# Kernel tuning notes

Hardware: AMD Instinct MI355X
Metric: run time of the kernel (lower is better)

The kernel has to match this reference:

```python
import jax, jax.numpy as jnp
import numpy as np
from jax import lax

N, C, H, W = 32, 256, 56, 56
SHIFT = 2  # p_5_1_0, frozen random.randint(-3,3)

def setup_inputs() -> dict:
    key = jax.random.key(0)
    k1, k2, k3 = jax.random.split(key, 3)
    x = jax.random.normal(k1, (N, C, H, W), dtype=jnp.float32)
    w6 = jax.random.normal(k2, (C, 1), dtype=jnp.float32) * 0.1  # trunc_normal(std=0.1) approx
    w7 = jax.random.normal(k3, (C, C * 25), dtype=jnp.float32) * (1.0 / np.sqrt(C * 25))
    return {"x": x, "w6": w6, "w7": w7}

def reference(x, w6, w7):
    # t_1: max over width -> (n,c,h)
    t1 = jnp.max(x, axis=3)
    # t_3/t_4: relu then tanh
    t4 = jnp.tanh(jax.nn.relu(x))
    # t_5: roll along height axis
    t5 = jnp.roll(x, SHIFT, axis=2)
    # t_6: einsum 'abcd,be->aecd' with e=1 -> (n,h,w)
    t6 = jnp.einsum('nchw,c->nhw', t4, w6[:, 0])
    # t_2 + p_7: unfold(5x5, dilation=3, padding=6) + 1x1 conv == dilated 5x5 conv.
    # unfold channel ordering is c*25 + (kh*5+kw), so reshape to OIHW directly.
    conv_w = w7.reshape(C, C, 5, 5)
    t7 = lax.conv_general_dilated(
        x, conv_w, window_strides=(1, 1), padding=[(6, 6), (6, 6)],
        rhs_dilation=(3, 3), dimension_numbers=('NCHW', 'OIHW', 'NCHW'))
    t8 = x * t7
    # t_9: softmax over width of (n,h,w)
    t9 = jax.nn.softmax(t6, axis=2)
    t10 = t9[:, None, :, :] * t5
    t11 = t10 + t8
    return t1[:, :, :, None] - t11
```

## Files before the change

### kernel.cpp

```cpp
#include <hip/hip_runtime.h>
#include <hip/hip_bf16.h>
#include <math.h>

typedef __bf16 bf16x8 __attribute__((ext_vector_type(8)));
typedef short  s16x8  __attribute__((ext_vector_type(8)));
typedef short  s16x4  __attribute__((ext_vector_type(4)));
typedef float  f32x16 __attribute__((ext_vector_type(16)));
typedef unsigned short u16;

#define NN 32
#define CC 256
#define HH 56
#define WW 56
#define HP 68
#define XP2_BYTES 75759616ull
#define XP2_OFF 0ull
#define WT3_OFF 75759616ull
#define T1_OFF  79036416ull
#define T9_OFF  80871424ull

__device__ inline u16 f2bf(float f) {
    unsigned int u = __builtin_bit_cast(unsigned int, f);
    u = (u + 0x7fffu + ((u >> 16) & 1u)) >> 16;
    return (u16)u;
}

__device__ inline void gl_lds16(const char* g, char* l) {
    __builtin_amdgcn_global_load_lds(
        (const __attribute__((address_space(1))) unsigned int*)g,
        (__attribute__((address_space(3))) unsigned int*)l, 16, 0, 0);
}

__global__ void zero_halo(u16* __restrict__ xp2) {
    const int total = NN * 1488 * 32;
    int i = blockIdx.x * blockDim.x + threadIdx.x;
    const int stride = gridDim.x * blockDim.x;
    uint4 z; z.x = z.y = z.z = z.w = 0u;
    for (; i < total; i += stride) {
        int chunk = i & 31;
        int pid = i >> 5;
        int n = pid / 1488;
        int hp = pid - n * 1488;
        int row, col;
        if (hp < 816) { int r = hp / 68; col = hp - r * 68; row = (r < 6) ? r : r + 56; }
        else { int hq = hp - 816; int rr = hq / 12; int c12 = hq - rr * 12;
               row = 6 + rr; col = (c12 < 6) ? c12 : c12 + 56; }
        *(uint4*)((char*)xp2 + ((((size_t)n * HP + row) * HP + col) * 512) + chunk * 16) = z;
    }
}

__global__ __launch_bounds__(256)
void pack_w(const float* __restrict__ w7, u16* __restrict__ wt3) {
    int idx = blockIdx.x * 256 + threadIdx.x;
    int c_out = idx / 6400;
    int k = idx - c_out * 6400;
    int cin = k / 25;
    int tap = k - cin * 25;
    int kn = tap * 8 + (cin >> 5);
    int c5 = cin & 31;
    int ks = c5 >> 4, half = (c5 >> 3) & 1, j = c5 & 7;
    int lane = half * 32 + (c_out & 31);
    int rb = c_out >> 5;
    wt3[(size_t)kn * 8192 + ks * 4096 + rb * 512 + lane * 8 + j] = f2bf(w7[idx]);
}

__global__ __launch_bounds__(256)
void prep(const float* __restrict__ x, const float* __restrict__ w6,
          float* __restrict__ t1, float* __restrict__ t9,
          u16* __restrict__ xp2) {
    const int n = blockIdx.x / HH;
    const int h = blockIdx.x % HH;
    const int tid = threadIdx.x;
    const int lane = tid & 63;
    const int wid = tid >> 6;
    const int g16 = lane >> 4;
    const int wq  = lane & 15;
    const bool act = wq < 14;
    __shared__ u16 xbuf[64 * 60];
    __shared__ float sacc[16][56];
    const float* xrow = x + ((size_t)(n * CC) * HH + h) * WW;
    u16* dst = xp2 + (((size_t)n * HP + h + 6) * HP + 6) * CC;
    float a0 = 0.f, a1 = 0.f, a2 = 0.f, a3 = 0.f;
    for (int g = 0; g < 4; ++g) {
        if (g) __syncthreads();
#pragma unroll
        for (int it = 0; it < 4; ++it) {
            const int cl = wid * 16 + it * 4 + g16;
            const int c  = g * 64 + cl;
            float4 v = make_float4(0.f, 0.f, 0.f, 0.f);
            if (act) v = *(const float4*)(xrow + (size_t)c * (HH * WW) + wq * 4);
            if (act) {
                s16x4 pk;
                pk[0] = (short)f2bf(v.x); pk[1] = (short)f2bf(v.y);
                pk[2] = (short)f2bf(v.z); pk[3] = (short)f2bf(v.w);
                *(s16x4*)(xbuf + cl * 60 + wq * 4) = pk;
            }
            float m = act ? fmaxf(fmaxf(v.x, v.y), fmaxf(v.z, v.w)) : -INFINITY;
#pragma unroll
            for (int off = 8; off > 0; off >>= 1)
                m = fmaxf(m, __shfl_xor(m, off));
            if (wq == 0) t1[(size_t)(n * CC + c) * HH + h] = m;
            if (act) {
                const float wc = w6[c];
                a0 += wc * (1.f - 2.f * __builtin_amdgcn_rcpf(__expf(2.f * fmaxf(v.x, 0.f)) + 1.f));
                a1 += wc * (1.f - 2.f * __builtin_amdgcn_rcpf(__expf(2.f * fmaxf(v.y, 0.f)) + 1.f));
                a2 += wc * (1.f - 2.f * __builtin_amdgcn_rcpf(__expf(2.f * fmaxf(v.z, 0.f)) + 1.f));
                a3 += wc * (1.f - 2.f * __builtin_amdgcn_rcpf(__expf(2.f * fmaxf(v.w, 0.f)) + 1.f));
            }
        }
        __syncthreads();
        for (int id = tid; id < WW * 8; id += 256) {
            int p = id >> 3, ch8 = id & 7;
            s16x8 pk;
#pragma unroll
            for (int j = 0; j < 8; ++j)
                pk[j] = (short)xbuf[(ch8 * 8 + j) * 60 + p];
            *(s16x8*)(dst + (size_t)p * CC + g * 64 + ch8 * 8) = pk;
        }
    }
    if (act) {
        float* sl = sacc[wid * 4 + g16];
        sl[wq * 4 + 0] = a0; sl[wq * 4 + 1] = a1;
        sl[wq * 4 + 2] = a2; sl[wq * 4 + 3] = a3;
    }
    __syncthreads();
    if (wid == 0) {
        const bool valid = lane < WW;
        float s = 0.f;
        if (valid) {
#pragma unroll
            for (int gi = 0; gi < 16; ++gi) s += sacc[gi][lane];
        }
        float sm = valid ? s : -INFINITY;
        float mx = sm;
#pragma unroll
        for (int off = 32; off > 0; off >>= 1)
            mx = fmaxf(mx, __shfl_xor(mx, off));
        float e = valid ? expf(s - mx) : 0.f;
        float tot = e;
#pragma unroll
        for (int off = 32; off > 0; off >>= 1)
            tot += __shfl_xor(tot, off);
        if (valid) t9[((size_t)n * HH + h) * WW + lane] = e / tot;
    }
}

__global__ __launch_bounds__(512, 2)
void conv_main(const char* __restrict__ xp2b, const char* __restrict__ wt3b,
               const float* __restrict__ x, const float* __restrict__ t1,
               const float* __restrict__ t9, float* __restrict__ out) {
    extern __shared__ __align__(16) char smem[];
    const int bid = blockIdx.x;
    const int tile = (bid & 7) * 49 + (bid >> 3);
    const int tid  = threadIdx.x;
    const int wid  = tid >> 6;
    const int lane = tid & 63;
    const int l31 = lane & 31;
    const int lhi = lane >> 5;
    const int wr = wid >> 2;
    const int wc = wid & 3;

    unsigned vb;
    {
        int p = tile * 256 + wid * 32 + l31;
        int n = p / (HH * WW);
        int rem = p - n * (HH * WW);
        int hh = rem / WW;
        int ww = rem - hh * WW;
        vb = ((((unsigned)n * HP + hh + 6) * HP) + ww + 6) * 512 + lhi * 16;
    }

    auto stageA = [&](int tt, int ks) {
        const int kn = (tt < 200) ? tt : (tt - 200);
        const unsigned o = ks * 8192 + wid * 1024 + lane * 16;
        char* d = smem + (size_t)(tt & 3) * 32768 + o;
        const char* g = wt3b + (size_t)kn * 16384 + o;
        gl_lds16(g, d);
    };
    auto stageB = [&](int tt, int ks) {
        const int kn = (tt < 200) ? tt : (tt - 200);
        const int tp = kn >> 3, ch = kn & 7;
        const char* gb = xp2b +
            (ptrdiff_t)((tp / 5) * 3 - 6) * (HP * 512) +
            (ptrdiff_t)((tp % 5) * 3 - 6) * 512 + ch * 64 + ks * 32 + vb;
        char* d = smem + (size_t)(tt & 3) * 32768 + 16384
                  + ks * 8192 + wid * 1024 + lane * 16;
        gl_lds16(gb, d);
    };

    f32x16 acc[4][2];
#pragma unroll
    for (int mi = 0; mi < 4; ++mi)
#pragma unroll
        for (int nb = 0; nb < 2; ++nb)
#pragma unroll
            for (int r = 0; r < 16; ++r)
                acc[mi][nb][r] = 0.f;

    const int aoff = wr * 4096 + lane * 16;
    const int boff = 16384 + wc * 2048 + lane * 16;

#pragma unroll
    for (int tt = 0; tt < 3; ++tt) {
        stageA(tt, 0); stageB(tt, 0);
        stageA(tt, 1); stageB(tt, 1);
    }
    asm volatile("s_waitcnt vmcnt(8)" ::: "memory");
    __builtin_amdgcn_s_barrier();

    for (int t = 0; t < 200; ++t) {
        const char* bp = smem + (size_t)(t & 3) * 32768;
        bf16x8 av[4], bv[2];

#pragma unroll
        for (int ks = 0; ks < 2; ++ks) {
            stageA(t + 3, ks); stageB(t + 3, ks);
#pragma unroll
            for (int nb = 0; nb < 2; ++nb)
                bv[nb] = *(const bf16x8*)(const void*)(bp + boff + ks * 8192 + nb * 1024);
#pragma unroll
            for (int mi = 0; mi < 4; ++mi)
                av[mi] = *(const bf16x8*)(const void*)(bp + aoff + ks * 8192 + mi * 1024);
            __builtin_amdgcn_s_setprio(1);
#pragma unroll
            for (int mi = 0; mi < 4; ++mi)
#pragma unroll
                for (int nb = 0; nb < 2; ++nb)
                    acc[mi][nb] = __builtin_amdgcn_mfma_f32_32x32x16_bf16(
                        av[mi], bv[nb], acc[mi][nb], 0, 0, 0);
            __builtin_amdgcn_s_setprio(0);
        }
        asm volatile("s_waitcnt vmcnt(8)" ::: "memory");
        __builtin_amdgcn_s_barrier();
    }

#pragma unroll
    for (int nb = 0; nb < 2; ++nb) {
        const int p = tile * 256 + wc * 64 + nb * 32 + l31;
        const int n = p / (HH * WW);
        const int rem = p - n * (HH * WW);
        const int h = rem / WW;
        const int w = rem - h * WW;
        const float t9v = t9[((size_t)n * HH + h) * WW + w];
        const int hprev = (h >= 2) ? (h - 2) : (h + HH - 2);
#pragma unroll
        for (int mi = 0; mi < 4; ++mi) {
            const int c0 = wr * 128 + mi * 32 + 4 * lhi;
#pragma unroll
            for (int r = 0; r < 16; ++r) {
                const int c = c0 + (r & 3) + 8 * (r >> 2);
                const size_t rowi = (size_t)(n * CC + c) * HH;
                const float t1v = t1[rowi + h];
                const float xv = x[(rowi + h) * WW + w];
                const float xr = x[(rowi + hprev) * WW + w];
                out[(rowi + h) * WW + w] = t1v - (t9v * xr + xv * acc[mi][nb][r]);
            }
        }
    }
}

extern "C" void kernel_launch(void* const* d_in, const int* in_sizes, int n_in,
                              void* d_out, int out_size, void* d_ws, size_t ws_size,
                              hipStream_t stream) {
    const float* x  = (const float*)d_in[0];
    const float* w6 = (const float*)d_in[1];
    const float* w7 = (const float*)d_in[2];
    float* out = (float*)d_out;
    char* ws = (char*)d_ws;
    u16*   xp2 = (u16*)(ws + XP2_OFF);
    u16*   wt3 = (u16*)(ws + WT3_OFF);
    float* t1  = (float*)(ws + T1_OFF);
    float* t9  = (float*)(ws + T9_OFF);

    static bool lds_cfg_done = false;
    if (!lds_cfg_done) {
        (void)hipFuncSetAttribute((const void*)conv_main,
                                  hipFuncAttributeMaxDynamicSharedMemorySize,
                                  131072);
        lds_cfg_done = true;
    }

    zero_halo<<<dim3(1024), dim3(256), 0, stream>>>(xp2);
    pack_w<<<dim3(6400), dim3(256), 0, stream>>>(w7, wt3);
    prep<<<dim3(NN * HH), dim3(256), 0, stream>>>(x, w6, t1, t9, xp2);
    conv_main<<<dim3(392), dim3(512), 131072, stream>>>((const char*)xp2, (const char*)wt3,
                                                        x, t1, t9, out);
}
```

Baseline: 585.9 us.

## Use 64-channel K tiles with double-buffered, phase-split MFMA pipeline

Repacks the weights into 64-input-channel K tiles and doubles the per-stage LDS buffer to 64 KB with two buffers instead of four 32 KB ones, halving the outer iteration count. The main loop is split into four phases, one per M sub-block. Each phase loads A fragments, issues part of the next stage's global-to-LDS copies, and runs eight MFMAs between explicit barriers and sched_barriers. The goal is to cut loop and barrier overhead per FLOP and interleave loads with MFMAs more finely, at the cost of more barriers per iteration and higher LDS and register use.

New measurement: 586.4 us. No clear change (+0.1%).

```diff
diff --git a/kernel.cpp b/kernel.cpp
--- a/kernel.cpp
+++ b/kernel.cpp
@@ -56,12 +56,12 @@
     int k = idx - c_out * 6400;
     int cin = k / 25;
     int tap = k - cin * 25;
-    int kn = tap * 8 + (cin >> 5);
-    int c5 = cin & 31;
-    int ks = c5 >> 4, half = (c5 >> 3) & 1, j = c5 & 7;
-    int lane = half * 32 + (c_out & 31);
-    int rb = c_out >> 5;
-    wt3[(size_t)kn * 8192 + ks * 4096 + rb * 512 + lane * 8 + j] = f2bf(w7[idx]);
+    int ktile = tap * 4 + (cin >> 6);
+    int k64 = cin & 63;
+    int ks = k64 >> 4, lhi = (k64 >> 3) & 1, j = k64 & 7;
+    int lane = lhi * 32 + (c_out & 31);
+    int mi = (c_out >> 5) & 3, wr = c_out >> 7;
+    wt3[(size_t)ktile * 16384 + mi * 4096 + ks * 1024 + wr * 512 + lane * 8 + j] = f2bf(w7[idx]);
 }
 
 __global__ __launch_bounds__(256)
@@ -169,22 +169,21 @@
         int ww = rem - hh * WW;
         vb = ((((unsigned)n * HP + hh + 6) * HP) + ww + 6) * 512 + lhi * 16;
     }
-
-    auto stageA = [&](int tt, int ks) {
-        const int kn = (tt < 200) ? tt : (tt - 200);
-        const unsigned o = ks * 8192 + wid * 1024 + lane * 16;
-        char* d = smem + (size_t)(tt & 3) * 32768 + o;
-        const char* g = wt3b + (size_t)kn * 16384 + o;
+    const unsigned aS = (wid & 3) * 2048 + (wid >> 2) * 1024 + lane * 16;
+
+    auto stageA = [&](int t2, int mi) {
+        const int kt = (t2 < 100) ? t2 : (t2 - 100);
+        char* d = smem + (size_t)(t2 & 1) * 65536 + mi * 8192 + aS;
+        const char* g = wt3b + (size_t)kt * 32768 + mi * 8192 + aS;
         gl_lds16(g, d);
     };
-    auto stageB = [&](int tt, int ks) {
-        const int kn = (tt < 200) ? tt : (tt - 200);
-        const int tp = kn >> 3, ch = kn & 7;
+    auto stageB = [&](int t2, int ks) {
+        const int kt = (t2 < 100) ? t2 : (t2 - 100);
+        const int tap = kt >> 2, u = kt & 3;
         const char* gb = xp2b +
-            (ptrdiff_t)((tp / 5) * 3 - 6) * (HP * 512) +
-            (ptrdiff_t)((tp % 5) * 3 - 6) * 512 + ch * 64 + ks * 32 + vb;
-        char* d = smem + (size_t)(tt & 3) * 32768 + 16384
-                  + ks * 8192 + wid * 1024 + lane * 16;
+            (ptrdiff_t)((tap / 5) * 3 - 6) * (HP * 512) +
+            (ptrdiff_t)((tap % 5) * 3 - 6) * 512 + u * 128 + ks * 32 + vb;
+        char* d = smem + (size_t)(t2 & 1) * 65536 + 32768 + ks * 8192 + wid * 1024 + lane * 16;
         gl_lds16(gb, d);
     };
 
@@ -197,42 +196,65 @@
             for (int r = 0; r < 16; ++r)
                 acc[mi][nb][r] = 0.f;
 
-    const int aoff = wr * 4096 + lane * 16;
-    const int boff = 16384 + wc * 2048 + lane * 16;
-
-#pragma unroll
-    for (int tt = 0; tt < 3; ++tt) {
-        stageA(tt, 0); stageB(tt, 0);
-        stageA(tt, 1); stageB(tt, 1);
-    }
-    asm volatile("s_waitcnt vmcnt(8)" ::: "memory");
-    __builtin_amdgcn_s_barrier();
-
-    for (int t = 0; t < 200; ++t) {
-        const char* bp = smem + (size_t)(t & 3) * 32768;
-        bf16x8 av[4], bv[2];
-
-#pragma unroll
-        for (int ks = 0; ks < 2; ++ks) {
-            stageA(t + 3, ks); stageB(t + 3, ks);
-#pragma unroll
-            for (int nb = 0; nb < 2; ++nb)
-                bv[nb] = *(const bf16x8*)(const void*)(bp + boff + ks * 8192 + nb * 1024);
-#pragma unroll
-            for (int mi = 0; mi < 4; ++mi)
-                av[mi] = *(const bf16x8*)(const void*)(bp + aoff + ks * 8192 + mi * 1024);
-            __builtin_amdgcn_s_setprio(1);
-#pragma unroll
-            for (int mi = 0; mi < 4; ++mi)
-#pragma unroll
-                for (int nb = 0; nb < 2; ++nb)
-                    acc[mi][nb] = __builtin_amdgcn_mfma_f32_32x32x16_bf16(
-                        av[mi], bv[nb], acc[mi][nb], 0, 0, 0);
-            __builtin_amdgcn_s_setprio(0);
-        }
-        asm volatile("s_waitcnt vmcnt(8)" ::: "memory");
+    const int aoff = wr * 1024 + lane * 16;
+    const int boff = 32768 + wc * 2048 + lane * 16;
+
+    stageA(0, 0); stageA(0, 1); stageA(0, 2); stageA(0, 3);
+    stageB(0, 0); stageB(0, 1); stageB(0, 2); stageB(0, 3);
+    stageA(1, 0); stageA(1, 1); stageA(1, 2);
+    stageB(1, 0); stageB(1, 1); stageB(1, 2);
+
+#define PHASE_N(MI)                                                            \
+    {                                                                          \
+        _Pragma("unroll")                                                      \
+        for (int ks = 0; ks < 4; ++ks)                                         \
+            av[ks] = *(const bf16x8*)(const void*)(bp + aoff + MI * 8192 + ks * 2048); \
+        stageA(t + 2, MI - 1); stageB(t + 2, MI - 1);                          \
+        __builtin_amdgcn_s_barrier();                                          \
+        __builtin_amdgcn_sched_barrier(0);                                     \
+        __builtin_amdgcn_s_setprio(1);                                         \
+        _Pragma("unroll")                                                      \
+        for (int ks = 0; ks < 4; ++ks) {                                       \
+            acc[MI][0] = __builtin_amdgcn_mfma_f32_32x32x16_bf16(              \
+                av[ks], bv[0][ks], acc[MI][0], 0, 0, 0);                       \
+            acc[MI][1] = __builtin_amdgcn_mfma_f32_32x32x16_bf16(              \
+                av[ks], bv[1][ks], acc[MI][1], 0, 0, 0);                       \
+        }                                                                      \
+        __builtin_amdgcn_s_setprio(0);                                         \
+        __builtin_amdgcn_s_barrier();                                          \
+        __builtin_amdgcn_sched_barrier(0);                                     \
+    }
+
+    for (int t = 0; t < 100; ++t) {
+        const char* bp = smem + (size_t)(t & 1) * 65536;
+        bf16x8 av[4], bv[2][4];
+        asm volatile("s_waitcnt vmcnt(6)" ::: "memory");
         __builtin_amdgcn_s_barrier();
-    }
+        __builtin_amdgcn_sched_barrier(0);
+#pragma unroll
+        for (int ks = 0; ks < 4; ++ks) {
+            bv[0][ks] = *(const bf16x8*)(const void*)(bp + boff + ks * 8192);
+            bv[1][ks] = *(const bf16x8*)(const void*)(bp + boff + ks * 8192 + 1024);
+            av[ks]    = *(const bf16x8*)(const void*)(bp + aoff + ks * 2048);
+        }
+        stageA(t + 1, 3); stageB(t + 1, 3);
+        __builtin_amdgcn_s_setprio(1);
+#pragma unroll
+        for (int ks = 0; ks < 4; ++ks) {
+            acc[0][0] = __builtin_amdgcn_mfma_f32_32x32x16_bf16(
+                av[ks], bv[0][ks], acc[0][0], 0, 0, 0);
+            acc[0][1] = __builtin_amdgcn_mfma_f32_32x32x16_bf16(
+                av[ks], bv[1][ks], acc[0][1], 0, 0, 0);
+        }
+        __builtin_amdgcn_s_setprio(0);
+        __builtin_amdgcn_s_barrier();
+        __builtin_amdgcn_sched_barrier(0);
+        PHASE_N(1)
+        PHASE_N(2)
+        PHASE_N(3)
+    }
+#undef PHASE_N
+    asm volatile("s_waitcnt vmcnt(0)" ::: "memory");
 
 #pragma unroll
     for (int nb = 0; nb < 2; ++nb) {
```

## Shrink conv tile to 128x128 with 4 waves, 3-stage LDS ring, more blocks

Applied to the files above, without the earlier changes.

The implicit-GEMM conv tile drops from 256 output channels x 256 pixels with 8 waves to 128 channels x 128 pixels with 4 waves. The output-channel dimension is split into two groups per block, and the weight packing is reordered to match. The LDS pipeline goes from a 4-deep buffer of 32KB stages to a 3-deep ring of 16KB stages, and the grid grows from 392 to 1568 blocks. The aim is better occupancy and load balance across CUs with less LDS per block, at the cost of lower arithmetic intensity and more redundant loads of activations and weights from global memory.

Result: slower. 659.0 us (+12.5%).

```diff
diff --git a/kernel.cpp b/kernel.cpp
--- a/kernel.cpp
+++ b/kernel.cpp
@@ -58,10 +58,10 @@
     int tap = k - cin * 25;
     int kn = tap * 8 + (cin >> 5);
     int c5 = cin & 31;
-    int ks = c5 >> 4, half = (c5 >> 3) & 1, j = c5 & 7;
-    int lane = half * 32 + (c_out & 31);
-    int rb = c_out >> 5;
-    wt3[(size_t)kn * 8192 + ks * 4096 + rb * 512 + lane * 8 + j] = f2bf(w7[idx]);
+    int ks = c5 >> 4, lhi = (c5 >> 3) & 1, j = c5 & 7;
+    int lane = lhi * 32 + (c_out & 31);
+    int cg = c_out >> 7, rb = (c_out >> 5) & 3;
+    wt3[(size_t)kn * 8192 + cg * 4096 + ks * 2048 + rb * 512 + lane * 8 + j] = f2bf(w7[idx]);
 }
 
 __global__ __launch_bounds__(256)
@@ -145,98 +145,95 @@
     }
 }
 
-__global__ __launch_bounds__(512, 2)
+__global__ __launch_bounds__(256, 3)
 void conv_main(const char* __restrict__ xp2b, const char* __restrict__ wt3b,
                const float* __restrict__ x, const float* __restrict__ t1,
                const float* __restrict__ t9, float* __restrict__ out) {
     extern __shared__ __align__(16) char smem[];
     const int bid = blockIdx.x;
-    const int tile = (bid & 7) * 49 + (bid >> 3);
-    const int tid  = threadIdx.x;
-    const int wid  = tid >> 6;
+    const int blk = (bid & 7) * 196 + (bid >> 3);
+    const int cg  = blk & 1;
+    const int pt  = blk >> 1;
+    const int tid = threadIdx.x;
+    const int wid = tid >> 6;
     const int lane = tid & 63;
     const int l31 = lane & 31;
     const int lhi = lane >> 5;
-    const int wr = wid >> 2;
-    const int wc = wid & 3;
-
-    unsigned vb;
-    {
-        int p = tile * 256 + wid * 32 + l31;
+    const int wr = wid >> 1;
+    const int wc = wid & 1;
+
+    unsigned vb[2];
+#pragma unroll
+    for (int i = 0; i < 2; ++i) {
+        int p = pt * 128 + ((2 * wid + i) & 3) * 32 + l31;
         int n = p / (HH * WW);
         int rem = p - n * (HH * WW);
         int hh = rem / WW;
         int ww = rem - hh * WW;
-        vb = ((((unsigned)n * HP + hh + 6) * HP) + ww + 6) * 512 + lhi * 16;
-    }
-
-    auto stageA = [&](int tt, int ks) {
-        const int kn = (tt < 200) ? tt : (tt - 200);
-        const unsigned o = ks * 8192 + wid * 1024 + lane * 16;
-        char* d = smem + (size_t)(tt & 3) * 32768 + o;
-        const char* g = wt3b + (size_t)kn * 16384 + o;
-        gl_lds16(g, d);
+        vb[i] = ((((unsigned)n * HP + hh + 6) * HP) + ww + 6) * 512
+                + (wid >> 1) * 32 + lhi * 16;
+    }
+
+    auto stageA = [&](int t2, int bi, int i) {
+        const int kn = (t2 < 200) ? t2 : (t2 - 200);
+        const unsigned o = (2 * wid + i) * 1024 + lane * 16;
+        gl_lds16(wt3b + (size_t)kn * 16384 + cg * 8192 + o,
+                 smem + bi * 16384 + o);
     };
-    auto stageB = [&](int tt, int ks) {
-        const int kn = (tt < 200) ? tt : (tt - 200);
-        const int tp = kn >> 3, ch = kn & 7;
+    auto stageB = [&](int t2, int bi, int i) {
+        const int kn = (t2 < 200) ? t2 : (t2 - 200);
+        const int tap = kn >> 3, ch = kn & 7;
         const char* gb = xp2b +
-            (ptrdiff_t)((tp / 5) * 3 - 6) * (HP * 512) +
-            (ptrdiff_t)((tp % 5) * 3 - 6) * 512 + ch * 64 + ks * 32 + vb;
-        char* d = smem + (size_t)(tt & 3) * 32768 + 16384
-                  + ks * 8192 + wid * 1024 + lane * 16;
-        gl_lds16(gb, d);
+            (ptrdiff_t)((tap / 5) * 3 - 6) * (HP * 512) +
+            (ptrdiff_t)((tap % 5) * 3 - 6) * 512 + ch * 64 + vb[i];
+        gl_lds16(gb, smem + bi * 16384 + 8192 + (2 * wid + i) * 1024 + lane * 16);
     };
 
-    f32x16 acc[4][2];
-#pragma unroll
-    for (int mi = 0; mi < 4; ++mi)
+    f32x16 acc[2][2];
+#pragma unroll
+    for (int mi = 0; mi < 2; ++mi)
 #pragma unroll
         for (int nb = 0; nb < 2; ++nb)
 #pragma unroll
             for (int r = 0; r < 16; ++r)
                 acc[mi][nb][r] = 0.f;
 
-    const int aoff = wr * 4096 + lane * 16;
-    const int boff = 16384 + wc * 2048 + lane * 16;
-
-#pragma unroll
-    for (int tt = 0; tt < 3; ++tt) {
-        stageA(tt, 0); stageB(tt, 0);
-        stageA(tt, 1); stageB(tt, 1);
-    }
-    asm volatile("s_waitcnt vmcnt(8)" ::: "memory");
+    const int aoff = wr * 2048 + lane * 16;
+    const int boff = 8192 + wc * 2048 + lane * 16;
+
+    stageA(0, 0, 0); stageB(0, 0, 0); stageA(0, 0, 1); stageB(0, 0, 1);
+    stageA(1, 1, 0); stageB(1, 1, 0); stageA(1, 1, 1); stageB(1, 1, 1);
+    asm volatile("s_waitcnt vmcnt(4)" ::: "memory");
     __builtin_amdgcn_s_barrier();
 
+    int bc = 0, bs = 2;
     for (int t = 0; t < 200; ++t) {
-        const char* bp = smem + (size_t)(t & 3) * 32768;
-        bf16x8 av[4], bv[2];
-
+        const char* bp = smem + bc * 16384;
+        bf16x8 av0, av1, bv0, bv1;
 #pragma unroll
         for (int ks = 0; ks < 2; ++ks) {
-            stageA(t + 3, ks); stageB(t + 3, ks);
-#pragma unroll
-            for (int nb = 0; nb < 2; ++nb)
-                bv[nb] = *(const bf16x8*)(const void*)(bp + boff + ks * 8192 + nb * 1024);
-#pragma unroll
-            for (int mi = 0; mi < 4; ++mi)
-                av[mi] = *(const bf16x8*)(const void*)(bp + aoff + ks * 8192 + mi * 1024);
+            stageA(t + 2, bs, ks); stageB(t + 2, bs, ks);
+            av0 = *(const bf16x8*)(const void*)(bp + aoff + ks * 4096);
+            av1 = *(const bf16x8*)(const void*)(bp + aoff + ks * 4096 + 1024);
+            bv0 = *(const bf16x8*)(const void*)(bp + boff + ks * 4096);
+            bv1 = *(const bf16x8*)(const void*)(bp + boff + ks * 4096 + 1024);
             __builtin_amdgcn_s_setprio(1);
-#pragma unroll
-            for (int mi = 0; mi < 4; ++mi)
-#pragma unroll
-                for (int nb = 0; nb < 2; ++nb)
-                    acc[mi][nb] = __builtin_amdgcn_mfma_f32_32x32x16_bf16(
-                        av[mi], bv[nb], acc[mi][nb], 0, 0, 0);
+            acc[0][0] = __builtin_amdgcn_mfma_f32_32x32x16_bf16(av0, bv0, acc[0][0], 0, 0, 0);
+            acc[0][1] = __builtin_amdgcn_mfma_f32_32x32x16_bf16(av0, bv1, acc[0][1], 0, 0, 0);
+            acc[1][0] = __builtin_amdgcn_mfma_f32_32x32x16_bf16(av1, bv0, acc[1][0], 0, 0, 0);
+            acc[1][1] = __builtin_amdgcn_mfma_f32_32x32x16_bf16(av1, bv1, acc[1][1], 0, 0, 0);
             __builtin_amdgcn_s_setprio(0);
         }
-        asm volatile("s_waitcnt vmcnt(8)" ::: "memory");
+        asm volatile("s_waitcnt vmcnt(4)" ::: "memory");
         __builtin_amdgcn_s_barrier();
-    }
+        bc = (bc == 2) ? 0 : bc + 1;
+        bs = (bs == 2) ? 0 : bs + 1;
+    }
+    asm volatile("s_waitcnt vmcnt(0)" ::: "memory");
 
 #pragma unroll
     for (int nb = 0; nb < 2; ++nb) {
-        const int p = tile * 256 + wc * 64 + nb * 32 + l31;
+        const int p = pt * 128 + wc * 64 + nb * 32 + l31;
         const int n = p / (HH * WW);
         const int rem = p - n * (HH * WW);
         const int h = rem / WW;
@@ -244,8 +241,8 @@
         const float t9v = t9[((size_t)n * HH + h) * WW + w];
         const int hprev = (h >= 2) ? (h - 2) : (h + HH - 2);
 #pragma unroll
-        for (int mi = 0; mi < 4; ++mi) {
-            const int c0 = wr * 128 + mi * 32 + 4 * lhi;
+        for (int mi = 0; mi < 2; ++mi) {
+            const int c0 = cg * 128 + wr * 64 + mi * 32 + 4 * lhi;
 #pragma unroll
             for (int r = 0; r < 16; ++r) {
                 const int c = c0 + (r & 3) + 8 * (r >> 2);
@@ -276,13 +273,13 @@
     if (!lds_cfg_done) {
         (void)hipFuncSetAttribute((const void*)conv_main,
                                   hipFuncAttributeMaxDynamicSharedMemorySize,
-                                  131072);
+                                  49152);
         lds_cfg_done = true;
     }
 
     zero_halo<<<dim3(1024), dim3(256), 0, stream>>>(xp2);
     pack_w<<<dim3(6400), dim3(256), 0, stream>>>(w7, wt3);
     prep<<<dim3(NN * HH), dim3(256), 0, stream>>>(x, w6, t1, t9, xp2);
-    conv_main<<<dim3(392), dim3(512), 131072, stream>>>((const char*)xp2, (const char*)wt3,
+    conv_main<<<dim3(1568), dim3(256), 49152, stream>>>((const char*)xp2, (const char*)wt3,
                                                         x, t1, t9, out);
 }
```
